# Kernel tuning notes

Hardware: AMD Instinct MI355X
Metric: run time of the kernel (lower is better)

The kernel has to match this reference:

```python
import jax, jax.numpy as jnp
import numpy as np

N, E, C1, E2, C2, B = 30000, 400000, 15000, 100000, 7500, 16
FV, FE, NC = 6, 3, 10


def _lin(k, i, o):
    kw, kb = jax.random.split(k)
    s = 1.0 / np.sqrt(i)
    w = jax.random.uniform(kw, (i, o), jnp.float32, -s, s)
    b = jax.random.uniform(kb, (o,), jnp.float32, -s, s)
    return w, b


def setup_inputs() -> dict:
    key = jax.random.key(0)
    ks = jax.random.split(key, 20)
    inp = {}
    inp["x"] = jax.random.normal(ks[0], (N, FV), jnp.float32)
    inp["edge_attr"] = jax.random.uniform(ks[1], (E, FE), jnp.float32)
    inp["pos"] = jax.random.uniform(ks[2], (N, 3), jnp.float32)
    inp["edge_index"] = jax.random.randint(ks[3], (2, E), 0, N)
    inp["batch"] = jnp.sort(jax.random.randint(ks[4], (N,), 0, B))
    inp["cluster1"] = jax.random.randint(ks[5], (N,), 0, C1)
    inp["edge_index2"] = jax.random.randint(ks[6], (2, E2), 0, C1)
    inp["cluster2"] = jax.random.randint(ks[7], (C1,), 0, C2)
    inp["w1a"], inp["b1a"] = _lin(ks[8], FE, 25)
    inp["w1b"], inp["b1b"] = _lin(ks[9], 25, 32 * FV)
    inp["root1"] = jax.random.normal(ks[10], (FV, 32), jnp.float32) / np.sqrt(FV)
    inp["bias1"] = jnp.zeros((32,), jnp.float32)
    inp["w2a"], inp["b2a"] = _lin(ks[11], 3, 25)
    inp["w2b"], inp["b2b"] = _lin(ks[12], 25, 32 * 64)
    inp["root2"] = jax.random.normal(ks[13], (32, 64), jnp.float32) / np.sqrt(32)
    inp["bias2"] = jnp.zeros((64,), jnp.float32)
    inp["fc1_w"], inp["fc1_b"] = _lin(ks[14], 64, 128)
    inp["fc2_w"], inp["fc2_b"] = _lin(ks[15], 128, NC)
    return inp


def _seg_mean(v, idx, n):
    s = jax.ops.segment_sum(v, idx, num_segments=n)
    c = jax.ops.segment_sum(jnp.ones(idx.shape, v.dtype), idx, num_segments=n)
    return s / jnp.maximum(c, 1.0)[:, None]


def _seg_max(v, idx, n):
    m = jax.ops.segment_max(v, idx, num_segments=n)
    return jnp.where(jnp.isfinite(m), m, 0.0)  # empty clusters -> 0


def _nnconv(x, src, dst, ea, wa, ba, wb, bb, root, bias, n, ci, co):
    # per-edge weight matrix from edge MLP: [E, ci, co]
    W = (jax.nn.relu(ea @ wa + ba) @ wb + bb).reshape(-1, ci, co)
    msg = jnp.einsum('ei,eio->eo', x[src], W)  # gather + per-edge matmul
    return _seg_mean(msg, dst, n) + x @ root + bias  # scatter-mean + root


def _cartesian(pos, src, dst):
    cart = pos[src] - pos[dst]
    return cart / (2.0 * jnp.max(jnp.abs(cart))) + 0.5  # T.Cartesian(norm=True)


def reference(x, edge_attr, pos, w1a, b1a, w1b, b1b, root1, bias1,
              w2a, b2a, w2b, b2b, root2, bias2, fc1_w, fc1_b, fc2_w, fc2_b,
              edge_index, batch, cluster1, edge_index2, cluster2):
    src1, dst1 = edge_index[0], edge_index[1]
    x1 = jax.nn.elu(_nnconv(x, src1, dst1, edge_attr, w1a, b1a, w1b, b1b,
                            root1, bias1, N, FV, 32))
    # max_pool with precomputed graclus cluster assignment
    xp = _seg_max(x1, cluster1, C1)
    posp = _seg_mean(pos, cluster1, C1)
    batchp = jnp.maximum(jax.ops.segment_max(batch, cluster1, num_segments=C1), 0)
    src2, dst2 = edge_index2[0], edge_index2[1]
    ea2 = _cartesian(posp, src2, dst2)
    x2 = jax.nn.elu(_nnconv(xp, src2, dst2, ea2, w2a, b2a, w2b, b2b,
                            root2, bias2, C1, 32, 64))
    # max_pool_x with second cluster assignment
    x3 = _seg_max(x2, cluster2, C2)
    batch2 = jnp.maximum(jax.ops.segment_max(batchp, cluster2, num_segments=C2), 0)
    g = _seg_mean(x3, batch2, B)  # global mean pool -> [B, 64]
    h = jax.nn.elu(g @ fc1_w + fc1_b)
    # dropout is identity in eval mode
    return jax.nn.log_softmax(h @ fc2_w + fc2_b, axis=1)
```

## Files before the change

kernel.cpp:

```cpp
#include <hip/hip_runtime.h>
#include <hip/hip_bf16.h>

#define Nn 30000
#define Ee 400000
#define C1n 15000
#define E2n 100000
#define C2n 7500
#define Bb 16

#define OFF_XPKEY   0
#define OFF_POSSUM  480000
#define OFF_CNTC1   525000
#define OFF_BPMAX   540000
#define OFF_X3KEY   555000
#define OFF_B2MAX   1035000
#define OFF_GSUM    1042500
#define OFF_GCNT    1043524
#define OFF_MAXABS  1043540
#define OFF_DEG1    1043544
#define OFF_FILL1   1073544
#define OFF_DEG2    1103544
#define OFF_FILL2   1118544
#define ZERO_ELEMS  1133544
#define OFF_RP1     1133544
#define OFF_RP2     1163548
#define OFF_POSP    1178552
#define OFF_XP      1223552
#define OFF_W1T     1703552
#define OFF_W2T     1707136
#define OFF_EA1R    1735808
#define OFF_C2R     3335808

typedef __attribute__((ext_vector_type(8))) short short8;
typedef __attribute__((ext_vector_type(4))) float f32x4;

__device__ __forceinline__ unsigned fkey(float f) {
    unsigned u = __float_as_uint(f);
    return (u >> 31) ? ~u : (u | 0x80000000u);
}
__device__ __forceinline__ float funkey(unsigned k) {
    unsigned u = (k >> 31) ? (k ^ 0x80000000u) : ~k;
    return __uint_as_float(u);
}
__device__ __forceinline__ float elu(float a) { return a > 0.f ? a : expm1f(a); }

__device__ __forceinline__ unsigned short f2bf(float f) {
    unsigned u = __float_as_uint(f);
    unsigned lsb = (u >> 16) & 1u;
    u += 0x7fffu + lsb;
    return (unsigned short)(u >> 16);
}

__global__ void hist_kernel(const int* __restrict__ ei, const int* __restrict__ ei2,
                            unsigned* __restrict__ deg1, unsigned* __restrict__ deg2) {
    int t = blockIdx.x * 256 + threadIdx.x;
    if (t < Ee) {
        atomicAdd(&deg1[ei[Ee + t]], 1u);
    } else if (t < Ee + E2n) {
        int e = t - Ee;
        atomicAdd(&deg2[ei2[E2n + e]], 1u);
    }
}

__global__ __launch_bounds__(1024) void scan_both(
    const unsigned* __restrict__ deg1, unsigned* __restrict__ rp1,
    const unsigned* __restrict__ deg2, unsigned* __restrict__ rp2) {
    const unsigned* deg; unsigned* rp; int n;
    if (blockIdx.x == 0) { deg = deg1; rp = rp1; n = Nn; }
    else                 { deg = deg2; rp = rp2; n = C1n; }
    __shared__ unsigned ps[1024];
    const int t = threadIdx.x;
    const int chunk = (n + 1023) / 1024;
    const int lo = t * chunk;
    const int hi = (lo + chunk < n) ? lo + chunk : n;
    unsigned s = 0;
    for (int i = lo; i < hi; ++i) s += deg[i];
    ps[t] = s;
    __syncthreads();
    for (int off = 1; off < 1024; off <<= 1) {
        unsigned v = (t >= off) ? ps[t - off] : 0u;
        __syncthreads();
        ps[t] += v;
        __syncthreads();
    }
    unsigned run = (t > 0) ? ps[t - 1] : 0u;
    if (t == 0) rp[0] = 0u;
    for (int i = lo; i < hi; ++i) { run += deg[i]; rp[i + 1] = run; }
}

__global__ void scatter1(const float* __restrict__ ea, const int* __restrict__ ei,
                         const unsigned* __restrict__ rp1, unsigned* __restrict__ fill1,
                         float4* __restrict__ EA1R) {
    int e = blockIdx.x * 256 + threadIdx.x;
    if (e >= Ee) return;
    int d = ei[Ee + e];
    unsigned p = rp1[d] + atomicAdd(&fill1[d], 1u);
    int src = ei[e];
    EA1R[p] = make_float4(ea[e * 3], ea[e * 3 + 1], ea[e * 3 + 2], __int_as_float(src));
}

__global__ void wt_kernel(const float* __restrict__ w1b, const float* __restrict__ b1b,
                          const float* __restrict__ root1, const float* __restrict__ bias1,
                          const float* __restrict__ w2b, const float* __restrict__ b2b,
                          const float* __restrict__ root2, const float* __restrict__ bias2,
                          unsigned short* __restrict__ W1T, unsigned short* __restrict__ W2T) {
    int t = blockIdx.x * 256 + threadIdx.x;
    if (t < 32 * 224) {
        int col = t / 224, p = t % 224;
        float v = 0.f;
        if (p < 208) {
            int k = p >> 3, i = p & 7;
            if (i < 6) v = (k < 25) ? w1b[k * 192 + i * 32 + col] : b1b[i * 32 + col];
        }
        else if (p < 214)  { v = root1[(p - 208) * 32 + col]; }
        else if (p == 214) { v = bias1[col]; }
        W1T[t] = f2bf(v);
    } else {
        int u = t - 32 * 224;
        if (u < 64 * 896) {
            int col = u / 896, p = u % 896;
            float v;
            if (p < 800)       { int k = p / 32, i = p % 32; v = w2b[k * 2048 + i * 64 + col]; }
            else if (p < 832)  { int i = p - 800; v = b2b[i * 64 + col]; }
            else if (p < 864)  { v = root2[(p - 832) * 64 + col]; }
            else if (p == 864) { v = bias2[col]; }
            else v = 0.f;
            W2T[u] = f2bf(v);
        }
    }
}

__global__ __launch_bounds__(256, 8) void g1conv1(
    const float* __restrict__ x, const float4* __restrict__ EA1R,
    const unsigned* __restrict__ rp1,
    const float* __restrict__ w1a, const float* __restrict__ b1a,
    const unsigned short* __restrict__ W1T,
    const float* __restrict__ pos, const int* __restrict__ batch, const int* __restrict__ cl1,
    unsigned* __restrict__ xpkey, float* __restrict__ possum,
    float* __restrict__ cntc1, int* __restrict__ bpmax) {
    __shared__ unsigned short As[16][232];
    const int tid = threadIdx.x;
    const int w = tid >> 6;
    const int l = tid & 63;
    const int m = l & 15, q = l >> 4;
    const int i8 = l & 7;
    const int kq = l >> 3;
    float wa0 = 0.f, wa1 = 0.f, wa2 = 0.f, ba0 = 0.f;
    if (l < 25) { wa0 = w1a[l]; wa1 = w1a[25 + l]; wa2 = w1a[50 + l]; ba0 = b1a[l]; }
    const int ntiles = Nn / 16;
    for (int tile = blockIdx.x; tile < ntiles; tile += gridDim.x) {
        const int base = tile * 16;
#pragma unroll
        for (int s4 = 0; s4 < 4; ++s4) {
            const int row = w * 4 + s4;
            const int d = base + row;
            const unsigned e0 = rp1[d], e1 = rp1[d + 1];
            float acc0 = 0.f, acc1 = 0.f, acc2 = 0.f, acc3 = 0.f;
            unsigned p = e0;
            for (; p + 4 <= e1; p += 4) {
                float4 ev[4];
#pragma unroll
                for (int b = 0; b < 4; ++b) ev[b] = EA1R[p + b];
                float xm[4];
#pragma unroll
                for (int b = 0; b < 4; ++b) {
                    const int sb = __float_as_int(ev[b].w) * 6;
                    xm[b] = (i8 < 6) ? x[sb + i8] : 0.f;
                }
#pragma unroll
                for (int b = 0; b < 4; ++b) {
                    float a = ba0 + ev[b].x * wa0 + ev[b].y * wa1 + ev[b].z * wa2;
                    float hown = (l == 25) ? 1.f : fmaxf(a, 0.f);
                    acc0 += __shfl(hown, kq, 64) * xm[b];
                    acc1 += __shfl(hown, 8 + kq, 64) * xm[b];
                    acc2 += __shfl(hown, 16 + kq, 64) * xm[b];
                    acc3 += __shfl(hown, 24 + kq, 64) * xm[b];
                }
            }
            for (; p < e1; ++p) {
                float4 ev = EA1R[p];
                const int sb = __float_as_int(ev.w) * 6;
                float xm = (i8 < 6) ? x[sb + i8] : 0.f;
                float a = ba0 + ev.x * wa0 + ev.y * wa1 + ev.z * wa2;
                float hown = (l == 25) ? 1.f : fmaxf(a, 0.f);
                acc0 += __shfl(hown, kq, 64) * xm;
                acc1 += __shfl(hown, 8 + kq, 64) * xm;
                acc2 += __shfl(hown, 16 + kq, 64) * xm;
                acc3 += __shfl(hown, 24 + kq, 64) * xm;
            }
            const float dinv = 1.f / fmaxf((float)(e1 - e0), 1.f);
            As[row][l] = f2bf(acc0 * dinv);
            As[row][64 + l] = f2bf(acc1 * dinv);
            As[row][128 + l] = f2bf(acc2 * dinv);
            if (l < 16) {
                As[row][192 + l] = f2bf(acc3 * dinv);
                float tail;
                if (l < 6)       tail = x[d * 6 + l];
                else if (l == 6) tail = 1.f;
                else             tail = 0.f;
                As[row][208 + l] = f2bf(tail);
            }
        }
        __syncthreads();
        if (w < 2) {
            f32x4 acc = {0.f, 0.f, 0.f, 0.f};
#pragma unroll
            for (int s = 0; s < 7; ++s) {
                short8 av = *reinterpret_cast<const short8*>(&As[m][s * 32 + q * 8]);
                short8 bv = *reinterpret_cast<const short8*>(&W1T[(w * 16 + m) * 224 + s * 32 + q * 8]);
                acc = __builtin_amdgcn_mfma_f32_16x16x32_bf16(av, bv, acc, 0, 0, 0);
            }
#pragma unroll
            for (int r = 0; r < 4; ++r) {
                const int row = base + q * 4 + r;
                const int c = cl1[row];
                float v = elu(acc[r]);
                atomicMax(&xpkey[c * 32 + w * 16 + m], fkey(v));
            }
        } else if (w == 2) {
            if (l < 16) {
                const int row = base + l;
                const int c = cl1[row];
#pragma unroll
                for (int j = 0; j < 3; ++j) atomicAdd(&possum[c * 3 + j], pos[row * 3 + j]);
                atomicAdd(&cntc1[c], 1.f);
                atomicMax(&bpmax[c], batch[row]);
            }
        }
        __syncthreads();
    }
}

__global__ void pool1_final(const unsigned* __restrict__ xpkey, const float* __restrict__ possum,
                            const float* __restrict__ cntc1, float* __restrict__ xp,
                            float* __restrict__ posp) {
    int t = blockIdx.x * 256 + threadIdx.x;
    if (t >= C1n * 32) return;
    int c = t >> 5, o = t & 31;
    unsigned k = xpkey[t];
    xp[t] = k ? funkey(k) : 0.f;
    if (o < 3) posp[c * 3 + o] = possum[c * 3 + o] / fmaxf(cntc1[c], 1.f);
}

__global__ void scatter2(const float* __restrict__ posp, const int* __restrict__ ei2,
                         const unsigned* __restrict__ rp2, unsigned* __restrict__ fill2,
                         float4* __restrict__ C2R, unsigned* __restrict__ maxabs) {
    int e = blockIdx.x * 256 + threadIdx.x;
    float mx = 0.f;
    if (e < E2n) {
        int s = ei2[e], d = ei2[E2n + e];
        float c0 = posp[s * 3]     - posp[d * 3];
        float c1 = posp[s * 3 + 1] - posp[d * 3 + 1];
        float c2 = posp[s * 3 + 2] - posp[d * 3 + 2];
        mx = fmaxf(fmaxf(fabsf(c0), fabsf(c1)), fabsf(c2));
        unsigned p = rp2[d] + atomicAdd(&fill2[d], 1u);
        C2R[p] = make_float4(c0, c1, c2, __int_as_float(s));
    }
#pragma unroll
    for (int off = 32; off > 0; off >>= 1) mx = fmaxf(mx, __shfl_xor(mx, off));
    if ((threadIdx.x & 63) == 0) atomicMax(maxabs, __float_as_uint(mx));
}

__global__ __launch_bounds__(512, 6) void g2conv2(
    const float* __restrict__ xp, const float4* __restrict__ C2R,
    const unsigned* __restrict__ maxabs, const unsigned* __restrict__ rp2,
    const float* __restrict__ w2a, const float* __restrict__ b2a,
    const unsigned short* __restrict__ W2T,
    const int* __restrict__ cl2, const int* __restrict__ bpmax,
    unsigned* __restrict__ x3key, int* __restrict__ b2max) {
    __shared__ unsigned short As[16][904];
    const int tid = threadIdx.x;
    const int w = tid >> 6;
    const int l = tid & 63;
    const int m = l & 15, q = l >> 4;
    const int i = l & 31, hp = l >> 5;
    float wa0 = 0.f, wa1 = 0.f, wa2 = 0.f, ba0 = 0.f;
    if (l < 25) { wa0 = w2a[l]; wa1 = w2a[25 + l]; wa2 = w2a[50 + l]; ba0 = b2a[l]; }
    const float inv = 0.5f / __uint_as_float(maxabs[0]);
    const int ntiles = (C1n + 15) / 16;
    for (int tile = blockIdx.x; tile < ntiles; tile += gridDim.x) {
        const int base = tile * 16;
#pragma unroll
        for (int s2 = 0; s2 < 2; ++s2) {
            const int row = w * 2 + s2;
            const int d = base + row;
            if (d < C1n) {
                const unsigned e0 = rp2[d], e1 = rp2[d + 1];
                float acc[13];
#pragma unroll
                for (int r = 0; r < 13; ++r) acc[r] = 0.f;
                unsigned p = e0;
                for (; p + 4 <= e1; p += 4) {
                    float4 cv[4];
#pragma unroll
                    for (int b = 0; b < 4; ++b) cv[b] = C2R[p + b];
                    float xv[4];
#pragma unroll
                    for (int b = 0; b < 4; ++b)
                        xv[b] = xp[__float_as_int(cv[b].w) * 32 + i];
#pragma unroll
                    for (int b = 0; b < 4; ++b) {
                        float a = ba0 + (cv[b].x * inv + 0.5f) * wa0 + (cv[b].y * inv + 0.5f) * wa1
                                      + (cv[b].z * inv + 0.5f) * wa2;
                        float hown = (l == 25) ? 1.f : fmaxf(a, 0.f);
#pragma unroll
                        for (int r = 0; r < 13; ++r)
                            acc[r] += __shfl(hown, 2 * r + hp, 64) * xv[b];
                    }
                }
                for (; p < e1; ++p) {
                    float4 cv = C2R[p];
                    float xv = xp[__float_as_int(cv.w) * 32 + i];
                    float a = ba0 + (cv.x * inv + 0.5f) * wa0 + (cv.y * inv + 0.5f) * wa1
                                  + (cv.z * inv + 0.5f) * wa2;
                    float hown = (l == 25) ? 1.f : fmaxf(a, 0.f);
#pragma unroll
                    for (int r = 0; r < 13; ++r)
                        acc[r] += __shfl(hown, 2 * r + hp, 64) * xv;
                }
                const float dinv = 1.f / fmaxf((float)(e1 - e0), 1.f);
#pragma unroll
                for (int r = 0; r < 13; ++r) As[row][r * 64 + l] = f2bf(acc[r] * dinv);
                As[row][832 + l] = f2bf((l < 32) ? xp[d * 32 + l] : (l == 32 ? 1.f : 0.f));
            } else {
#pragma unroll
                for (int r = 0; r < 13; ++r) As[row][r * 64 + l] = 0;
                As[row][832 + l] = 0;
            }
        }
        __syncthreads();
        if (w < 4) {
            f32x4 a4 = {0.f, 0.f, 0.f, 0.f};
#pragma unroll 4
            for (int s = 0; s < 28; ++s) {
                short8 av = *reinterpret_cast<const short8*>(&As[m][s * 32 + q * 8]);
                short8 bv = *reinterpret_cast<const short8*>(&W2T[(w * 16 + m) * 896 + s * 32 + q * 8]);
                a4 = __builtin_amdgcn_mfma_f32_16x16x32_bf16(av, bv, a4, 0, 0, 0);
            }
#pragma unroll
            for (int r = 0; r < 4; ++r) {
                const int row = base + q * 4 + r;
                if (row < C1n) {
                    const int c2 = cl2[row];
                    float v = elu(a4[r]);
                    atomicMax(&x3key[c2 * 64 + w * 16 + m], fkey(v));
                }
            }
        } else if (w == 4) {
            if (l < 16) {
                const int row = base + l;
                if (row < C1n) atomicMax(&b2max[cl2[row]], bpmax[row]);
            }
        }
        __syncthreads();
    }
}

__global__ __launch_bounds__(256) void gacc_kernel(
    const unsigned* __restrict__ x3key, const int* __restrict__ b2max,
    float* __restrict__ gsum, float* __restrict__ gcnt) {
    __shared__ float ls[Bb * 64];
    __shared__ float lc[Bb];
    const int t = threadIdx.x;
    for (int i = t; i < Bb * 64; i += 256) ls[i] = 0.f;
    if (t < Bb) lc[t] = 0.f;
    __syncthreads();
    const int o = t & 63;
    const int cs = t >> 6;
    for (int c = blockIdx.x * 4 + cs; c < C2n; c += gridDim.x * 4) {
        int b = b2max[c];
        unsigned k = x3key[c * 64 + o];
        float v = k ? funkey(k) : 0.f;
        atomicAdd(&ls[b * 64 + o], v);
        if (o == 0) atomicAdd(&lc[b], 1.f);
    }
    __syncthreads();
    for (int i = t; i < Bb * 64; i += 256) {
        float v = ls[i];
        if (v != 0.f) atomicAdd(&gsum[i], v);
    }
    if (t < Bb) {
        float v = lc[t];
        if (v != 0.f) atomicAdd(&gcnt[t], v);
    }
}

__global__ void head_kernel(const float* __restrict__ gsum, const float* __restrict__ gcnt,
                            const float* __restrict__ fc1w, const float* __restrict__ fc1b,
                            const float* __restrict__ fc2w, const float* __restrict__ fc2b,
                            float* __restrict__ out) {
    __shared__ float g[16 * 64];
    __shared__ float hb[16 * 128];
    __shared__ float lg[16 * 10];
    __shared__ float rowm[16];
    int t = threadIdx.x;
    for (int idx = t; idx < 16 * 64; idx += 256) {
        int b = idx >> 6;
        g[idx] = gsum[idx] / fmaxf(gcnt[b], 1.f);
    }
    __syncthreads();
    for (int idx = t; idx < 16 * 128; idx += 256) {
        int b = idx >> 7, j = idx & 127;
        float a = fc1b[j];
        for (int i = 0; i < 64; ++i) a += g[b * 64 + i] * fc1w[i * 128 + j];
        hb[idx] = elu(a);
    }
    __syncthreads();
    for (int idx = t; idx < 160; idx += 256) {
        int b = idx / 10, c = idx % 10;
        float a = fc2b[c];
        for (int i = 0; i < 128; ++i) a += hb[b * 128 + i] * fc2w[i * 10 + c];
        lg[idx] = a;
    }
    __syncthreads();
    if (t < 16) {
        float m = -1e30f;
        for (int c = 0; c < 10; ++c) m = fmaxf(m, lg[t * 10 + c]);
        float s = 0.f;
        for (int c = 0; c < 10; ++c) s += expf(lg[t * 10 + c] - m);
        rowm[t] = m + logf(s);
    }
    __syncthreads();
    for (int idx = t; idx < 160; idx += 256) out[idx] = lg[idx] - rowm[idx / 10];
}

extern "C" void kernel_launch(void* const* d_in, const int* in_sizes, int n_in,
                              void* d_out, int out_size, void* d_ws, size_t ws_size,
                              hipStream_t stream) {
    const float* x     = (const float*)d_in[0];
    const float* ea    = (const float*)d_in[1];
    const float* pos   = (const float*)d_in[2];
    const int*   ei    = (const int*)d_in[3];
    const int*   batch = (const int*)d_in[4];
    const int*   cl1   = (const int*)d_in[5];
    const int*   ei2   = (const int*)d_in[6];
    const int*   cl2   = (const int*)d_in[7];
    const float* w1a   = (const float*)d_in[8];
    const float* b1a   = (const float*)d_in[9];
    const float* w1b   = (const float*)d_in[10];
    const float* b1b   = (const float*)d_in[11];
    const float* root1 = (const float*)d_in[12];
    const float* bias1 = (const float*)d_in[13];
    const float* w2a   = (const float*)d_in[14];
    const float* b2a   = (const float*)d_in[15];
    const float* w2b   = (const float*)d_in[16];
    const float* b2b   = (const float*)d_in[17];
    const float* root2 = (const float*)d_in[18];
    const float* bias2 = (const float*)d_in[19];
    const float* fc1w  = (const float*)d_in[20];
    const float* fc1b  = (const float*)d_in[21];
    const float* fc2w  = (const float*)d_in[22];
    const float* fc2b  = (const float*)d_in[23];
    float* out = (float*)d_out;

    float* ws = (float*)d_ws;
    unsigned* xpkey  = (unsigned*)(ws + OFF_XPKEY);
    float*    possum = ws + OFF_POSSUM;
    float*    cntc1  = ws + OFF_CNTC1;
    int*      bpmax  = (int*)(ws + OFF_BPMAX);
    unsigned* x3key  = (unsigned*)(ws + OFF_X3KEY);
    int*      b2max  = (int*)(ws + OFF_B2MAX);
    float*    gsum   = ws + OFF_GSUM;
    float*    gcnt   = ws + OFF_GCNT;
    unsigned* maxabs = (unsigned*)(ws + OFF_MAXABS);
    unsigned* deg1   = (unsigned*)(ws + OFF_DEG1);
    unsigned* fill1  = (unsigned*)(ws + OFF_FILL1);
    unsigned* deg2   = (unsigned*)(ws + OFF_DEG2);
    unsigned* fill2  = (unsigned*)(ws + OFF_FILL2);
    unsigned* rp1    = (unsigned*)(ws + OFF_RP1);
    unsigned* rp2    = (unsigned*)(ws + OFF_RP2);
    float*    posp   = ws + OFF_POSP;
    float*    xp     = ws + OFF_XP;
    unsigned short* W1T = (unsigned short*)(ws + OFF_W1T);
    unsigned short* W2T = (unsigned short*)(ws + OFF_W2T);
    float4*   EA1R  = (float4*)(ws + OFF_EA1R);
    float4*   C2R   = (float4*)(ws + OFF_C2R);

    hipMemsetAsync(ws, 0, (size_t)ZERO_ELEMS * 4, stream);

    wt_kernel<<<252, 256, 0, stream>>>(w1b, b1b, root1, bias1, w2b, b2b, root2, bias2, W1T, W2T);
    hist_kernel<<<(Ee + E2n + 255) / 256, 256, 0, stream>>>(ei, ei2, deg1, deg2);
    scan_both<<<2, 1024, 0, stream>>>(deg1, rp1, deg2, rp2);
    scatter1<<<(Ee + 255) / 256, 256, 0, stream>>>(ea, ei, rp1, fill1, EA1R);
    g1conv1<<<1875, 256, 0, stream>>>(x, EA1R, rp1, w1a, b1a, W1T, pos, batch, cl1,
                                      xpkey, possum, cntc1, bpmax);
    pool1_final<<<(C1n * 32 + 255) / 256, 256, 0, stream>>>(xpkey, possum, cntc1, xp, posp);
    scatter2<<<(E2n + 255) / 256, 256, 0, stream>>>(posp, ei2, rp2, fill2, C2R, maxabs);
    g2conv2<<<938, 512, 0, stream>>>(xp, C2R, maxabs, rp2, w2a, b2a, W2T, cl2, bpmax,
                                     x3key, b2max);
    gacc_kernel<<<32, 256, 0, stream>>>(x3key, b2max, gsum, gcnt);
    head_kernel<<<1, 256, 0, stream>>>(gsum, gcnt, fc1w, fc1b, fc2w, fc2b, out);
}
```

Measured before the change: 349.0 us.

## Merge edge-loop remainders into masked unrolled loop and shrink g2conv2 blocks to 256

Both conv kernels drop the separate scalar remainder loop and run the 4-wide unrolled edge loop with clamped indices and masked gathers, so tail edges use the batched loads. g2conv2 moves from 512-thread blocks, each wave gathering two rows, to 256-thread blocks where each wave gathers four rows and all four waves run the MFMA stage. The batch-max atomic is folded into the gather phase, one per row. This removes idle waves during the MFMA phase and the remainder-loop code, but does redundant masked work on short segments and halves gather parallelism per block.

```diff
diff --git a/kernel.cpp b/kernel.cpp
--- a/kernel.cpp
+++ b/kernel.cpp
@@ -156,16 +156,18 @@
             const int d = base + row;
             const unsigned e0 = rp1[d], e1 = rp1[d + 1];
             float acc0 = 0.f, acc1 = 0.f, acc2 = 0.f, acc3 = 0.f;
-            unsigned p = e0;
-            for (; p + 4 <= e1; p += 4) {
+            for (unsigned p = e0; p < e1; p += 4) {
                 float4 ev[4];
-#pragma unroll
-                for (int b = 0; b < 4; ++b) ev[b] = EA1R[p + b];
                 float xm[4];
+#pragma unroll
+                for (int b = 0; b < 4; ++b) {
+                    const unsigned pp = (p + b < e1) ? p + b : e1 - 1;
+                    ev[b] = EA1R[pp];
+                }
 #pragma unroll
                 for (int b = 0; b < 4; ++b) {
                     const int sb = __float_as_int(ev[b].w) * 6;
-                    xm[b] = (i8 < 6) ? x[sb + i8] : 0.f;
+                    xm[b] = (i8 < 6 && p + b < e1) ? x[sb + i8] : 0.f;
                 }
 #pragma unroll
                 for (int b = 0; b < 4; ++b) {
@@ -176,17 +178,6 @@
                     acc2 += __shfl(hown, 16 + kq, 64) * xm[b];
                     acc3 += __shfl(hown, 24 + kq, 64) * xm[b];
                 }
-            }
-            for (; p < e1; ++p) {
-                float4 ev = EA1R[p];
-                const int sb = __float_as_int(ev.w) * 6;
-                float xm = (i8 < 6) ? x[sb + i8] : 0.f;
-                float a = ba0 + ev.x * wa0 + ev.y * wa1 + ev.z * wa2;
-                float hown = (l == 25) ? 1.f : fmaxf(a, 0.f);
-                acc0 += __shfl(hown, kq, 64) * xm;
-                acc1 += __shfl(hown, 8 + kq, 64) * xm;
-                acc2 += __shfl(hown, 16 + kq, 64) * xm;
-                acc3 += __shfl(hown, 24 + kq, 64) * xm;
             }
             const float dinv = 1.f / fmaxf((float)(e1 - e0), 1.f);
             As[row][l] = f2bf(acc0 * dinv);
@@ -261,7 +252,7 @@
     if ((threadIdx.x & 63) == 0) atomicMax(maxabs, __float_as_uint(mx));
 }
 
-__global__ __launch_bounds__(512, 6) void g2conv2(
+__global__ __launch_bounds__(256, 5) void g2conv2(
     const float* __restrict__ xp, const float4* __restrict__ C2R,
     const unsigned* __restrict__ maxabs, const unsigned* __restrict__ rp2,
     const float* __restrict__ w2a, const float* __restrict__ b2a,
@@ -281,23 +272,25 @@
     for (int tile = blockIdx.x; tile < ntiles; tile += gridDim.x) {
         const int base = tile * 16;
 #pragma unroll
-        for (int s2 = 0; s2 < 2; ++s2) {
-            const int row = w * 2 + s2;
+        for (int s4 = 0; s4 < 4; ++s4) {
+            const int row = w * 4 + s4;
             const int d = base + row;
             if (d < C1n) {
                 const unsigned e0 = rp2[d], e1 = rp2[d + 1];
                 float acc[13];
 #pragma unroll
                 for (int r = 0; r < 13; ++r) acc[r] = 0.f;
-                unsigned p = e0;
-                for (; p + 4 <= e1; p += 4) {
+                for (unsigned p = e0; p < e1; p += 4) {
                     float4 cv[4];
-#pragma unroll
-                    for (int b = 0; b < 4; ++b) cv[b] = C2R[p + b];
                     float xv[4];
 #pragma unroll
+                    for (int b = 0; b < 4; ++b) {
+                        const unsigned pp = (p + b < e1) ? p + b : e1 - 1;
+                        cv[b] = C2R[pp];
+                    }
+#pragma unroll
                     for (int b = 0; b < 4; ++b)
-                        xv[b] = xp[__float_as_int(cv[b].w) * 32 + i];
+                        xv[b] = (p + b < e1) ? xp[__float_as_int(cv[b].w) * 32 + i] : 0.f;
 #pragma unroll
                     for (int b = 0; b < 4; ++b) {
                         float a = ba0 + (cv[b].x * inv + 0.5f) * wa0 + (cv[b].y * inv + 0.5f) * wa1
@@ -308,20 +301,11 @@
                             acc[r] += __shfl(hown, 2 * r + hp, 64) * xv[b];
                     }
                 }
-                for (; p < e1; ++p) {
-                    float4 cv = C2R[p];
-                    float xv = xp[__float_as_int(cv.w) * 32 + i];
-                    float a = ba0 + (cv.x * inv + 0.5f) * wa0 + (cv.y * inv + 0.5f) * wa1
-                                  + (cv.z * inv + 0.5f) * wa2;
-                    float hown = (l == 25) ? 1.f : fmaxf(a, 0.f);
-#pragma unroll
-                    for (int r = 0; r < 13; ++r)
-                        acc[r] += __shfl(hown, 2 * r + hp, 64) * xv;
-                }
                 const float dinv = 1.f / fmaxf((float)(e1 - e0), 1.f);
 #pragma unroll
                 for (int r = 0; r < 13; ++r) As[row][r * 64 + l] = f2bf(acc[r] * dinv);
                 As[row][832 + l] = f2bf((l < 32) ? xp[d * 32 + l] : (l == 32 ? 1.f : 0.f));
+                if (l == 0) atomicMax(&b2max[cl2[d]], bpmax[d]);
             } else {
 #pragma unroll
                 for (int r = 0; r < 13; ++r) As[row][r * 64 + l] = 0;
@@ -329,7 +313,7 @@
             }
         }
         __syncthreads();
-        if (w < 4) {
+        {
             f32x4 a4 = {0.f, 0.f, 0.f, 0.f};
 #pragma unroll 4
             for (int s = 0; s < 28; ++s) {
@@ -345,11 +329,6 @@
                     float v = elu(a4[r]);
                     atomicMax(&x3key[c2 * 64 + w * 16 + m], fkey(v));
                 }
-            }
-        } else if (w == 4) {
-            if (l < 16) {
-                const int row = base + l;
-                if (row < C1n) atomicMax(&b2max[cl2[row]], bpmax[row]);
             }
         }
         __syncthreads();
@@ -486,7 +465,7 @@
                                       xpkey, possum, cntc1, bpmax);
     pool1_final<<<(C1n * 32 + 255) / 256, 256, 0, stream>>>(xpkey, possum, cntc1, xp, posp);
     scatter2<<<(E2n + 255) / 256, 256, 0, stream>>>(posp, ei2, rp2, fill2, C2R, maxabs);
-    g2conv2<<<938, 512, 0, stream>>>(xp, C2R, maxabs, rp2, w2a, b2a, W2T, cl2, bpmax,
+    g2conv2<<<938, 256, 0, stream>>>(xp, C2R, maxabs, rp2, w2a, b2a, W2T, cl2, bpmax,
                                      x3key, b2max);
     gacc_kernel<<<32, 256, 0, stream>>>(x3key, b2max, gsum, gcnt);
     head_kernel<<<1, 256, 0, stream>>>(gsum, gcnt, fc1w, fc1b, fc2w, fc2b, out);
```

After: 340.3 us. -2.5%, faster.
